# Performance work log

Measured on AMD Instinct MI355X. Metric: run time of the kernel, lower is better.

The kernel has to match this reference:

```python
import jax, jax.numpy as jnp
import numpy as np

EPS = 1e-8


def _layer_norm(x, w, b):
    mu = jnp.mean(x, axis=-1, keepdims=True)
    var = jnp.mean((x - mu) ** 2, axis=-1, keepdims=True)
    return (x - mu) * jax.lax.rsqrt(var + EPS) * w + b


def setup_inputs() -> dict:
    key = jax.random.key(0)
    k1, k2, k3 = jax.random.split(key, 3)
    B, S, D = 8, 2048, 1024
    return {
        "x_real": jax.random.normal(k1, (B, S, D), dtype=jnp.float32),
        "x_imag": jax.random.normal(k2, (B, S, D), dtype=jnp.float32),
        "phase_matrix": jax.random.normal(k3, (D, D), dtype=jnp.float32) * 0.02,
        "coherence_factor": jnp.ones((1,), dtype=jnp.float32) * 0.1,
        "ln_weight": jnp.ones((D,), dtype=jnp.float32),
        "ln_bias": jnp.zeros((D,), dtype=jnp.float32),
    }


def reference(x_real, x_imag, phase_matrix, coherence_factor, ln_weight, ln_bias):
    D = x_real.shape[-1]
    # coherence = mean_{i,j} cos(phi_i - phi_j) over the last dim pairwise;
    # exact trig identity: sum_{i,j} cos(phi_i-phi_j) = (sum cos)^2 + (sum sin)^2
    phases = jnp.arctan2(x_imag + EPS, x_real + EPS)          # [B,S,D]
    sc = jnp.sum(jnp.cos(phases), axis=-1, keepdims=True)      # [B,S,1]
    ss = jnp.sum(jnp.sin(phases), axis=-1, keepdims=True)      # [B,S,1]
    coherence = (sc * sc + ss * ss) / (D * D)                  # [B,S,1]

    # phase rotation driven by GEMM
    phase_adjustment = jnp.einsum('bsd,de->bse', x_real, phase_matrix)
    phase_adjustment = phase_adjustment * coherence_factor * (1.0 - coherence)
    c, s = jnp.cos(phase_adjustment), jnp.sin(phase_adjustment)
    new_real = x_real * c - x_imag * s
    new_imag = x_real * s + x_imag * c

    # unit-modulus normalization
    norm = jnp.sqrt(new_real ** 2 + new_imag ** 2 + EPS)
    new_real = new_real / norm
    new_imag = new_imag / norm

    return (_layer_norm(new_real, ln_weight, ln_bias),
            _layer_norm(new_imag, ln_weight, ln_bias))
```

## Files before the change

### kernel.cpp

```cpp
#include <hip/hip_runtime.h>
#include <hip/hip_fp16.h>

#define DEV __device__ __forceinline__

typedef __bf16 bf16x8 __attribute__((ext_vector_type(8)));
typedef float f32x4 __attribute__((ext_vector_type(4)));
typedef short s16x8 __attribute__((ext_vector_type(8)));
typedef unsigned short u16;

static constexpr int D = 1024;
static constexpr int M = 16384;
static constexpr int R = 32;
static constexpr float EPS = 1e-8f;
static constexpr int PAD = 1028;

static constexpr int SMEM_BYTES = 136192;
static constexpr int RED_OFF = 131584;
static constexpr int STATS_OFF = 135680;

DEV u16 f2bf(float f) {
  union { float f; unsigned u; } v; v.f = f;
  unsigned u = v.u;
  return (u16)((u + 0x7FFFu + ((u >> 16) & 1u)) >> 16);
}

union H2x4 { s16x8 v; __half2 h[4]; };

__global__ __launch_bounds__(256) void k_prep(const float* __restrict__ pm,
                                              u16* __restrict__ bt) {
  __shared__ float t[32][33];
  int bx = blockIdx.x * 32, by = blockIdx.y * 32;
  int tx = threadIdx.x, ty = threadIdx.y;
#pragma unroll
  for (int j = 0; j < 32; j += 8)
    t[ty + j][tx] = pm[(size_t)(by + ty + j) * D + bx + tx];
  __syncthreads();
#pragma unroll
  for (int j = 0; j < 32; j += 8) {
    int col = bx + ty + j, k = by + tx;
    int kk = k >> 5, nh = col >> 9, cb = (col >> 4) & 31, c15 = col & 15;
    int kg = (k >> 3) & 3, je = k & 7;
    bt[(size_t)(kk * 2 + nh) * 16384 + (size_t)((cb * 64 + kg * 16 + c15) * 8 + je)] =
        f2bf(t[tx][ty + j]);
  }
}

__global__ __launch_bounds__(512, 1) void k_fused(
    const float* __restrict__ xr, const float* __restrict__ xi,
    const u16* __restrict__ bt, const float* __restrict__ cfp,
    const float* __restrict__ lw, const float* __restrict__ lb,
    float* __restrict__ outR, float* __restrict__ outI) {
  __shared__ __align__(16) unsigned char smem[SMEM_BYTES];
  u16* A_lds = (u16*)smem;
  __half2* stash = (__half2*)smem;
  float* red = (float*)(smem + RED_OFF);
  float* stats = (float*)(smem + STATS_OFF);

  const int tid = threadIdx.x;
  const int lane = tid & 63;
  const int l15 = lane & 15, l4 = lane >> 4;
  const int wv = tid >> 6;
  const size_t row0 = (size_t)blockIdx.x * R;
  const float cfv = cfp[0];

  {
    int row = tid >> 4;
    int s16 = tid & 15;
    const float* src = xr + (row0 + row) * D;
#pragma unroll
    for (int it = 0; it < 4; ++it)
#pragma unroll
      for (int h = 0; h < 2; ++h) {
        int kgl = it * 32 + s16 * 2 + h;
        f32x4 a = *(const f32x4*)(src + kgl * 8);
        f32x4 b = *(const f32x4*)(src + kgl * 8 + 4);
        s16x8 v;
        v[0] = (short)f2bf(a.x); v[1] = (short)f2bf(a.y);
        v[2] = (short)f2bf(a.z); v[3] = (short)f2bf(a.w);
        v[4] = (short)f2bf(b.x); v[5] = (short)f2bf(b.y);
        v[6] = (short)f2bf(b.z); v[7] = (short)f2bf(b.w);
        int kk = kgl >> 2, kg = kgl & 3;
        int u = kk * 128 + (row >> 4) * 64 + kg * 16 + ((row & 15) ^ (kk & 15));
        *(s16x8*)&A_lds[u * 8] = v;
      }
  }
  __syncthreads();

  f32x4 acc[2][8] = {};

  auto loadA = [&](int kk, bf16x8 (&af)[2]) {
#pragma unroll
    for (int rb = 0; rb < 2; ++rb) {
      int u = kk * 128 + rb * 64 + l4 * 16 + (l15 ^ (kk & 15));
      af[rb] = __builtin_bit_cast(bf16x8, *(const s16x8*)&A_lds[u * 8]);
    }
  };
  auto loadB4 = [&](int s, bf16x8 (&b)[4]) {
    const u16* p = bt + (size_t)s * 16384 + (size_t)(wv * 4) * 512 + (size_t)lane * 8;
#pragma unroll
    for (int nf = 0; nf < 4; ++nf)
      b[nf] = __builtin_bit_cast(bf16x8, *(const s16x8*)(p + nf * 512));
  };
  auto step4 = [&](bf16x8 (&a)[2], bf16x8 (&b)[4], int nh) {
    __builtin_amdgcn_s_setprio(1);
#pragma unroll
    for (int nf = 0; nf < 4; ++nf) {
      acc[0][nh * 4 + nf] =
          __builtin_amdgcn_mfma_f32_16x16x32_bf16(a[0], b[nf], acc[0][nh * 4 + nf], 0, 0, 0);
      acc[1][nh * 4 + nf] =
          __builtin_amdgcn_mfma_f32_16x16x32_bf16(a[1], b[nf], acc[1][nh * 4 + nf], 0, 0, 0);
    }
    __builtin_amdgcn_s_setprio(0);
  };

  {
    bf16x8 a[2], b0v[4], b1v[4];
    loadB4(0, b0v);
    loadB4(1, b1v);
    for (int kk = 0; kk < 32; ++kk) {
      loadA(kk, a);
      step4(a, b0v, 0);
      if (kk < 31) loadB4(2 * kk + 2, b0v);
      step4(a, b1v, 1);
      if (kk < 31) loadB4(2 * kk + 3, b1v);
    }
  }
  __syncthreads();

  float sc8[8], ss8[8];
#pragma unroll
  for (int p = 0; p < 8; ++p) { sc8[p] = 0.f; ss8[p] = 0.f; }
#pragma unroll
  for (int rb = 0; rb < 2; ++rb)
#pragma unroll
    for (int i = 0; i < 4; ++i) {
      const int p = rb * 4 + i;
      const int row_l = rb * 16 + l4 * 4 + i;
      const float* ar = xr + (row0 + row_l) * D;
      const float* ai = xi + (row0 + row_l) * D;
#pragma unroll
      for (int q = 0; q < 8; ++q) {
        int col = (q >> 2) * 512 + wv * 64 + (q & 3) * 16 + l15;
        float a = ar[col], b = ai[col];
        float xe = a + EPS, ye = b + EPS;
        float inv = rsqrtf(xe * xe + ye * ye);
        sc8[p] += xe * inv;
        ss8[p] += ye * inv;
        stash[row_l * PAD + col] = __floats2half2_rn(a, b);
      }
    }
#pragma unroll
  for (int p = 0; p < 8; ++p)
#pragma unroll
    for (int d = 1; d < 16; d <<= 1) {
      sc8[p] += __shfl_xor(sc8[p], d, 64);
      ss8[p] += __shfl_xor(ss8[p], d, 64);
    }
  if (l15 == 0) {
#pragma unroll
    for (int rb = 0; rb < 2; ++rb)
#pragma unroll
      for (int i = 0; i < 4; ++i) {
        int p = rb * 4 + i, row_l = rb * 16 + l4 * 4 + i;
        red[(row_l * 8 + wv) * 4 + 0] = sc8[p];
        red[(row_l * 8 + wv) * 4 + 1] = ss8[p];
      }
  }
  __syncthreads();
  float srow[8];
#pragma unroll
  for (int rb = 0; rb < 2; ++rb)
#pragma unroll
    for (int i = 0; i < 4; ++i) {
      int p = rb * 4 + i, row_l = rb * 16 + l4 * 4 + i;
      float tsc = 0.f, tss = 0.f;
#pragma unroll
      for (int w8 = 0; w8 < 8; ++w8) {
        tsc += red[(row_l * 8 + w8) * 4 + 0];
        tss += red[(row_l * 8 + w8) * 4 + 1];
      }
      float coh = (tsc * tsc + tss * tss) * (1.0f / (1024.0f * 1024.0f));
      srow[p] = cfv * (1.0f - coh);
    }
  __syncthreads();

  float snr[8], sqr[8], sni[8], sqi[8];
#pragma unroll
  for (int p = 0; p < 8; ++p) { snr[p] = 0.f; sqr[p] = 0.f; sni[p] = 0.f; sqi[p] = 0.f; }
#pragma unroll
  for (int rb = 0; rb < 2; ++rb)
#pragma unroll
    for (int i = 0; i < 4; ++i) {
      const int p = rb * 4 + i;
      const int row_l = rb * 16 + l4 * 4 + i;
      const float sr = srow[p];
#pragma unroll
      for (int q = 0; q < 8; ++q) {
        int col = (q >> 2) * 512 + wv * 64 + (q & 3) * 16 + l15;
        float t = acc[rb][q][i] * sr;
        float t2 = t * t;
        float sn = t * (1.f + t2 * (-1.f / 6.f + t2 * (1.f / 120.f - t2 * (1.f / 5040.f))));
        float cs = 1.f + t2 * (-0.5f + t2 * (1.f / 24.f - t2 * (1.f / 720.f)));
        __half2 ab = stash[row_l * PAD + col];
        float a = __low2float(ab), b = __high2float(ab);
        float nr = a * cs - b * sn;
        float ni = a * sn + b * cs;
        float inv = rsqrtf(nr * nr + ni * ni + EPS);
        nr *= inv; ni *= inv;
        stash[row_l * PAD + col] = __floats2half2_rn(nr, ni);
        snr[p] += nr; sqr[p] += nr * nr;
        sni[p] += ni; sqi[p] += ni * ni;
      }
    }
#pragma unroll
  for (int p = 0; p < 8; ++p)
#pragma unroll
    for (int d = 1; d < 16; d <<= 1) {
      snr[p] += __shfl_xor(snr[p], d, 64);
      sqr[p] += __shfl_xor(sqr[p], d, 64);
      sni[p] += __shfl_xor(sni[p], d, 64);
      sqi[p] += __shfl_xor(sqi[p], d, 64);
    }
  if (l15 == 0) {
#pragma unroll
    for (int rb = 0; rb < 2; ++rb)
#pragma unroll
      for (int i = 0; i < 4; ++i) {
        int p = rb * 4 + i, row_l = rb * 16 + l4 * 4 + i;
        red[(row_l * 8 + wv) * 4 + 0] = snr[p];
        red[(row_l * 8 + wv) * 4 + 1] = sqr[p];
        red[(row_l * 8 + wv) * 4 + 2] = sni[p];
        red[(row_l * 8 + wv) * 4 + 3] = sqi[p];
      }
  }
  __syncthreads();
  if (wv == 0 && l15 == 0) {
#pragma unroll
    for (int rb = 0; rb < 2; ++rb)
#pragma unroll
      for (int i = 0; i < 4; ++i) {
        int row_l = rb * 16 + l4 * 4 + i;
        float s0 = 0.f, s1 = 0.f, s2 = 0.f, s3 = 0.f;
#pragma unroll
        for (int w8 = 0; w8 < 8; ++w8) {
          s0 += red[(row_l * 8 + w8) * 4 + 0];
          s1 += red[(row_l * 8 + w8) * 4 + 1];
          s2 += red[(row_l * 8 + w8) * 4 + 2];
          s3 += red[(row_l * 8 + w8) * 4 + 3];
        }
        float mu_r = s0 * (1.f / 1024.f);
        float mu_i = s2 * (1.f / 1024.f);
        stats[row_l * 4 + 0] = mu_r;
        stats[row_l * 4 + 1] = rsqrtf(s1 * (1.f / 1024.f) - mu_r * mu_r + EPS);
        stats[row_l * 4 + 2] = mu_i;
        stats[row_l * 4 + 3] = rsqrtf(s3 * (1.f / 1024.f) - mu_i * mu_i + EPS);
      }
  }
  __syncthreads();

  {
    int row = tid >> 4, cg = tid & 15;
    float mu_r = stats[row * 4 + 0], rd_r = stats[row * 4 + 1];
    float mu_i = stats[row * 4 + 2], rd_i = stats[row * 4 + 3];
    float* orp = outR + (row0 + row) * D;
    float* oip = outI + (row0 + row) * D;
#pragma unroll
    for (int v = 0; v < 16; ++v) {
      int col = v * 64 + cg * 4;
      H2x4 hv;
      hv.v = *(const s16x8*)&stash[row * PAD + col];
      f32x4 w4 = *(const f32x4*)(lw + col);
      f32x4 b4 = *(const f32x4*)(lb + col);
      f32x4 o_r, o_i;
#pragma unroll
      for (int j = 0; j < 4; ++j) {
        float nr = __low2float(hv.h[j]), ni = __high2float(hv.h[j]);
        o_r[j] = (nr - mu_r) * rd_r * w4[j] + b4[j];
        o_i[j] = (ni - mu_i) * rd_i * w4[j] + b4[j];
      }
      *(f32x4*)(orp + col) = o_r;
      *(f32x4*)(oip + col) = o_i;
    }
  }
}

extern "C" void kernel_launch(void* const* d_in, const int* in_sizes, int n_in,
                              void* d_out, int out_size, void* d_ws, size_t ws_size,
                              hipStream_t stream) {
  const float* xr = (const float*)d_in[0];
  const float* xi = (const float*)d_in[1];
  const float* pm = (const float*)d_in[2];
  const float* cf = (const float*)d_in[3];
  const float* lw = (const float*)d_in[4];
  const float* lb = (const float*)d_in[5];
  float* outR = (float*)d_out;
  float* outI = outR + (size_t)M * D;
  u16* bt = (u16*)d_ws;

  k_prep<<<dim3(32, 32), dim3(32, 8), 0, stream>>>(pm, bt);
  k_fused<<<M / R, 512, 0, stream>>>(xr, xi, bt, cf, lw, lb, outR, outI);
}
```

Before: 160.2 us.

## Halve row tile, stage B via async LDS loads, fuse coherence into A load

Shrinks the per-block row tile from 32 to 16 so LDS use drops to about 66KB, and raises launch bounds to allow several blocks per CU. The B operand is now copied cooperatively into shared memory with global_load_lds each k-step instead of being loaded straight into registers per wave. The coherence sums are computed while loading x for the bf16 A tile, so the separate fp16 stash pass over the inputs goes away; the stash now uses an XOR swizzle in place of padding. The cost is twice as many blocks each re-reading the full B matrix, and two barriers per half k-step with no double buffering of B.

```diff
diff --git a/kernel.cpp b/kernel.cpp
--- a/kernel.cpp
+++ b/kernel.cpp
@@ -10,18 +10,25 @@
 
 static constexpr int D = 1024;
 static constexpr int M = 16384;
-static constexpr int R = 32;
+static constexpr int R = 16;
 static constexpr float EPS = 1e-8f;
-static constexpr int PAD = 1028;
-
-static constexpr int SMEM_BYTES = 136192;
-static constexpr int RED_OFF = 131584;
-static constexpr int STATS_OFF = 135680;
+
+static constexpr int B_OFF = 32768;
+static constexpr int RED_OFF = 65536;
+static constexpr int STATS_OFF = 67584;
+static constexpr int SCALE_OFF = 67840;
+static constexpr int SMEM_BYTES = 67904;
 
 DEV u16 f2bf(float f) {
   union { float f; unsigned u; } v; v.f = f;
   unsigned u = v.u;
   return (u16)((u + 0x7FFFu + ((u >> 16) & 1u)) >> 16);
+}
+
+DEV void async_copy16(const void* g, void* l) {
+  __builtin_amdgcn_global_load_lds(
+      (const __attribute__((address_space(1))) void*)g,
+      (__attribute__((address_space(3))) void*)l, 16, 0, 0);
 }
 
 union H2x4 { s16x8 v; __half2 h[4]; };
@@ -45,16 +52,18 @@
   }
 }
 
-__global__ __launch_bounds__(512, 1) void k_fused(
+__global__ __launch_bounds__(512, 4) void k_fused(
     const float* __restrict__ xr, const float* __restrict__ xi,
     const u16* __restrict__ bt, const float* __restrict__ cfp,
     const float* __restrict__ lw, const float* __restrict__ lb,
     float* __restrict__ outR, float* __restrict__ outI) {
   __shared__ __align__(16) unsigned char smem[SMEM_BYTES];
   u16* A_lds = (u16*)smem;
+  u16* B_u16 = (u16*)(smem + B_OFF);
   __half2* stash = (__half2*)smem;
   float* red = (float*)(smem + RED_OFF);
   float* stats = (float*)(smem + STATS_OFF);
+  float* scale_s = (float*)(smem + SCALE_OFF);
 
   const int tid = threadIdx.x;
   const int lane = tid & 63;
@@ -64,211 +73,158 @@
   const float cfv = cfp[0];
 
   {
-    int row = tid >> 4;
-    int s16 = tid & 15;
-    const float* src = xr + (row0 + row) * D;
-#pragma unroll
-    for (int it = 0; it < 4; ++it)
-#pragma unroll
-      for (int h = 0; h < 2; ++h) {
-        int kgl = it * 32 + s16 * 2 + h;
-        f32x4 a = *(const f32x4*)(src + kgl * 8);
-        f32x4 b = *(const f32x4*)(src + kgl * 8 + 4);
-        s16x8 v;
-        v[0] = (short)f2bf(a.x); v[1] = (short)f2bf(a.y);
-        v[2] = (short)f2bf(a.z); v[3] = (short)f2bf(a.w);
-        v[4] = (short)f2bf(b.x); v[5] = (short)f2bf(b.y);
-        v[6] = (short)f2bf(b.z); v[7] = (short)f2bf(b.w);
-        int kk = kgl >> 2, kg = kgl & 3;
-        int u = kk * 128 + (row >> 4) * 64 + kg * 16 + ((row & 15) ^ (kk & 15));
-        *(s16x8*)&A_lds[u * 8] = v;
-      }
-  }
-  __syncthreads();
-
-  f32x4 acc[2][8] = {};
-
-  auto loadA = [&](int kk, bf16x8 (&af)[2]) {
-#pragma unroll
-    for (int rb = 0; rb < 2; ++rb) {
-      int u = kk * 128 + rb * 64 + l4 * 16 + (l15 ^ (kk & 15));
-      af[rb] = __builtin_bit_cast(bf16x8, *(const s16x8*)&A_lds[u * 8]);
-    }
-  };
-  auto loadB4 = [&](int s, bf16x8 (&b)[4]) {
-    const u16* p = bt + (size_t)s * 16384 + (size_t)(wv * 4) * 512 + (size_t)lane * 8;
-#pragma unroll
-    for (int nf = 0; nf < 4; ++nf)
-      b[nf] = __builtin_bit_cast(bf16x8, *(const s16x8*)(p + nf * 512));
-  };
-  auto step4 = [&](bf16x8 (&a)[2], bf16x8 (&b)[4], int nh) {
-    __builtin_amdgcn_s_setprio(1);
-#pragma unroll
-    for (int nf = 0; nf < 4; ++nf) {
-      acc[0][nh * 4 + nf] =
-          __builtin_amdgcn_mfma_f32_16x16x32_bf16(a[0], b[nf], acc[0][nh * 4 + nf], 0, 0, 0);
-      acc[1][nh * 4 + nf] =
-          __builtin_amdgcn_mfma_f32_16x16x32_bf16(a[1], b[nf], acc[1][nh * 4 + nf], 0, 0, 0);
-    }
-    __builtin_amdgcn_s_setprio(0);
-  };
+    int row = tid >> 5;
+    int s32 = tid & 31;
+    const float* xrp = xr + (row0 + row) * D;
+    const float* xip = xi + (row0 + row) * D;
+    float sc = 0.f, ss = 0.f;
+#pragma unroll
+    for (int it = 0; it < 4; ++it) {
+      int kgl = it * 32 + s32;
+      f32x4 a0 = *(const f32x4*)(xrp + kgl * 8);
+      f32x4 a1 = *(const f32x4*)(xrp + kgl * 8 + 4);
+      f32x4 b0 = *(const f32x4*)(xip + kgl * 8);
+      f32x4 b1 = *(const f32x4*)(xip + kgl * 8 + 4);
+      float fx[8] = {a0.x, a0.y, a0.z, a0.w, a1.x, a1.y, a1.z, a1.w};
+      float fy[8] = {b0.x, b0.y, b0.z, b0.w, b1.x, b1.y, b1.z, b1.w};
+      s16x8 v;
+#pragma unroll
+      for (int j = 0; j < 8; ++j) {
+        float x = fx[j] + EPS, y = fy[j] + EPS;
+        float inv = rsqrtf(x * x + y * y);
+        sc += x * inv;
+        ss += y * inv;
+        v[j] = (short)f2bf(fx[j]);
+      }
+      int kk = kgl >> 2, kg = kgl & 3;
+      int u = kk * 64 + kg * 16 + (row ^ (kk & 15));
+      *(s16x8*)&A_lds[u * 8] = v;
+    }
+    sc += __shfl_xor(sc, 1, 64); sc += __shfl_xor(sc, 2, 64);
+    sc += __shfl_xor(sc, 4, 64); sc += __shfl_xor(sc, 8, 64);
+    sc += __shfl_xor(sc, 16, 64);
+    ss += __shfl_xor(ss, 1, 64); ss += __shfl_xor(ss, 2, 64);
+    ss += __shfl_xor(ss, 4, 64); ss += __shfl_xor(ss, 8, 64);
+    ss += __shfl_xor(ss, 16, 64);
+    if (s32 == 0) {
+      float coh = (sc * sc + ss * ss) * (1.0f / (1024.0f * 1024.0f));
+      scale_s[row] = cfv * (1.0f - coh);
+    }
+  }
+  __syncthreads();
+
+  f32x4 acc[8] = {};
+
+  for (int kk = 0; kk < 32; ++kk) {
+    int ua = kk * 64 + l4 * 16 + (l15 ^ (kk & 15));
+    bf16x8 af = __builtin_bit_cast(bf16x8, *(const s16x8*)&A_lds[ua * 8]);
+#pragma unroll
+    for (int nh = 0; nh < 2; ++nh) {
+      const u16* src = bt + (size_t)(kk * 2 + nh) * 16384;
+#pragma unroll
+      for (int r = 0; r < 4; ++r) {
+        int off = (r * 8 + wv) * 512 + lane * 8;
+        async_copy16(src + off, B_u16 + off);
+      }
+      __syncthreads();
+      __builtin_amdgcn_s_setprio(1);
+#pragma unroll
+      for (int nf = 0; nf < 4; ++nf) {
+        int ub = (wv * 4 + nf) * 64 + l4 * 16 + l15;
+        bf16x8 bf = __builtin_bit_cast(bf16x8, *(const s16x8*)&B_u16[ub * 8]);
+        acc[nh * 4 + nf] =
+            __builtin_amdgcn_mfma_f32_16x16x32_bf16(af, bf, acc[nh * 4 + nf], 0, 0, 0);
+      }
+      __builtin_amdgcn_s_setprio(0);
+      __syncthreads();
+    }
+  }
+
+  float srow4[4];
+#pragma unroll
+  for (int i = 0; i < 4; ++i) srow4[i] = scale_s[l4 * 4 + i];
+
+  float s_r[4], q_r[4], s_i[4], q_i[4];
+#pragma unroll
+  for (int i = 0; i < 4; ++i) { s_r[i] = 0.f; q_r[i] = 0.f; s_i[i] = 0.f; q_i[i] = 0.f; }
+#pragma unroll
+  for (int i = 0; i < 4; ++i) {
+    const int row_l = l4 * 4 + i;
+    const float scl = srow4[i];
+    const float* ar = xr + (row0 + row_l) * D;
+    const float* ai = xi + (row0 + row_l) * D;
+#pragma unroll
+    for (int q = 0; q < 8; ++q) {
+      int col = (q >> 2) * 512 + wv * 64 + (q & 3) * 16 + l15;
+      float a = ar[col], b = ai[col];
+      float t = acc[q][i] * scl;
+      float t2 = t * t;
+      float sn = t * (1.f + t2 * (-1.f / 6.f + t2 * (1.f / 120.f - t2 * (1.f / 5040.f))));
+      float cs = 1.f + t2 * (-0.5f + t2 * (1.f / 24.f - t2 * (1.f / 720.f)));
+      float nr = a * cs - b * sn;
+      float ni = a * sn + b * cs;
+      float inv = rsqrtf(nr * nr + ni * ni + EPS);
+      nr *= inv; ni *= inv;
+      int colx = col ^ ((row_l & 3) << 4);
+      stash[row_l * 1024 + colx] = __floats2half2_rn(nr, ni);
+      s_r[i] += nr; q_r[i] += nr * nr;
+      s_i[i] += ni; q_i[i] += ni * ni;
+    }
+  }
+#pragma unroll
+  for (int i = 0; i < 4; ++i)
+#pragma unroll
+    for (int d = 1; d < 16; d <<= 1) {
+      s_r[i] += __shfl_xor(s_r[i], d, 64);
+      q_r[i] += __shfl_xor(q_r[i], d, 64);
+      s_i[i] += __shfl_xor(s_i[i], d, 64);
+      q_i[i] += __shfl_xor(q_i[i], d, 64);
+    }
+  if (l15 == 0) {
+#pragma unroll
+    for (int i = 0; i < 4; ++i) {
+      int row_l = l4 * 4 + i;
+      red[(row_l * 8 + wv) * 4 + 0] = s_r[i];
+      red[(row_l * 8 + wv) * 4 + 1] = q_r[i];
+      red[(row_l * 8 + wv) * 4 + 2] = s_i[i];
+      red[(row_l * 8 + wv) * 4 + 3] = q_i[i];
+    }
+  }
+  __syncthreads();
+  if (wv == 0 && l15 == 0) {
+#pragma unroll
+    for (int i = 0; i < 4; ++i) {
+      int row_l = l4 * 4 + i;
+      float s0 = 0.f, s1 = 0.f, s2 = 0.f, s3 = 0.f;
+#pragma unroll
+      for (int w8 = 0; w8 < 8; ++w8) {
+        s0 += red[(row_l * 8 + w8) * 4 + 0];
+        s1 += red[(row_l * 8 + w8) * 4 + 1];
+        s2 += red[(row_l * 8 + w8) * 4 + 2];
+        s3 += red[(row_l * 8 + w8) * 4 + 3];
+      }
+      float mu_r = s0 * (1.f / 1024.f);
+      float mu_i = s2 * (1.f / 1024.f);
+      stats[row_l * 4 + 0] = mu_r;
+      stats[row_l * 4 + 1] = rsqrtf(s1 * (1.f / 1024.f) - mu_r * mu_r + EPS);
+      stats[row_l * 4 + 2] = mu_i;
+      stats[row_l * 4 + 3] = rsqrtf(s3 * (1.f / 1024.f) - mu_i * mu_i + EPS);
+    }
+  }
+  __syncthreads();
 
   {
-    bf16x8 a[2], b0v[4], b1v[4];
-    loadB4(0, b0v);
-    loadB4(1, b1v);
-    for (int kk = 0; kk < 32; ++kk) {
-      loadA(kk, a);
-      step4(a, b0v, 0);
-      if (kk < 31) loadB4(2 * kk + 2, b0v);
-      step4(a, b1v, 1);
-      if (kk < 31) loadB4(2 * kk + 3, b1v);
-    }
-  }
-  __syncthreads();
-
-  float sc8[8], ss8[8];
-#pragma unroll
-  for (int p = 0; p < 8; ++p) { sc8[p] = 0.f; ss8[p] = 0.f; }
-#pragma unroll
-  for (int rb = 0; rb < 2; ++rb)
-#pragma unroll
-    for (int i = 0; i < 4; ++i) {
-      const int p = rb * 4 + i;
-      const int row_l = rb * 16 + l4 * 4 + i;
-      const float* ar = xr + (row0 + row_l) * D;
-      const float* ai = xi + (row0 + row_l) * D;
-#pragma unroll
-      for (int q = 0; q < 8; ++q) {
-        int col = (q >> 2) * 512 + wv * 64 + (q & 3) * 16 + l15;
-        float a = ar[col], b = ai[col];
-        float xe = a + EPS, ye = b + EPS;
-        float inv = rsqrtf(xe * xe + ye * ye);
-        sc8[p] += xe * inv;
-        ss8[p] += ye * inv;
-        stash[row_l * PAD + col] = __floats2half2_rn(a, b);
-      }
-    }
-#pragma unroll
-  for (int p = 0; p < 8; ++p)
-#pragma unroll
-    for (int d = 1; d < 16; d <<= 1) {
-      sc8[p] += __shfl_xor(sc8[p], d, 64);
-      ss8[p] += __shfl_xor(ss8[p], d, 64);
-    }
-  if (l15 == 0) {
-#pragma unroll
-    for (int rb = 0; rb < 2; ++rb)
-#pragma unroll
-      for (int i = 0; i < 4; ++i) {
-        int p = rb * 4 + i, row_l = rb * 16 + l4 * 4 + i;
-        red[(row_l * 8 + wv) * 4 + 0] = sc8[p];
-        red[(row_l * 8 + wv) * 4 + 1] = ss8[p];
-      }
-  }
-  __syncthreads();
-  float srow[8];
-#pragma unroll
-  for (int rb = 0; rb < 2; ++rb)
-#pragma unroll
-    for (int i = 0; i < 4; ++i) {
-      int p = rb * 4 + i, row_l = rb * 16 + l4 * 4 + i;
-      float tsc = 0.f, tss = 0.f;
-#pragma unroll
-      for (int w8 = 0; w8 < 8; ++w8) {
-        tsc += red[(row_l * 8 + w8) * 4 + 0];
-        tss += red[(row_l * 8 + w8) * 4 + 1];
-      }
-      float coh = (tsc * tsc + tss * tss) * (1.0f / (1024.0f * 1024.0f));
-      srow[p] = cfv * (1.0f - coh);
-    }
-  __syncthreads();
-
-  float snr[8], sqr[8], sni[8], sqi[8];
-#pragma unroll
-  for (int p = 0; p < 8; ++p) { snr[p] = 0.f; sqr[p] = 0.f; sni[p] = 0.f; sqi[p] = 0.f; }
-#pragma unroll
-  for (int rb = 0; rb < 2; ++rb)
-#pragma unroll
-    for (int i = 0; i < 4; ++i) {
-      const int p = rb * 4 + i;
-      const int row_l = rb * 16 + l4 * 4 + i;
-      const float sr = srow[p];
-#pragma unroll
-      for (int q = 0; q < 8; ++q) {
-        int col = (q >> 2) * 512 + wv * 64 + (q & 3) * 16 + l15;
-        float t = acc[rb][q][i] * sr;
-        float t2 = t * t;
-        float sn = t * (1.f + t2 * (-1.f / 6.f + t2 * (1.f / 120.f - t2 * (1.f / 5040.f))));
-        float cs = 1.f + t2 * (-0.5f + t2 * (1.f / 24.f - t2 * (1.f / 720.f)));
-        __half2 ab = stash[row_l * PAD + col];
-        float a = __low2float(ab), b = __high2float(ab);
-        float nr = a * cs - b * sn;
-        float ni = a * sn + b * cs;
-        float inv = rsqrtf(nr * nr + ni * ni + EPS);
-        nr *= inv; ni *= inv;
-        stash[row_l * PAD + col] = __floats2half2_rn(nr, ni);
-        snr[p] += nr; sqr[p] += nr * nr;
-        sni[p] += ni; sqi[p] += ni * ni;
-      }
-    }
-#pragma unroll
-  for (int p = 0; p < 8; ++p)
-#pragma unroll
-    for (int d = 1; d < 16; d <<= 1) {
-      snr[p] += __shfl_xor(snr[p], d, 64);
-      sqr[p] += __shfl_xor(sqr[p], d, 64);
-      sni[p] += __shfl_xor(sni[p], d, 64);
-      sqi[p] += __shfl_xor(sqi[p], d, 64);
-    }
-  if (l15 == 0) {
-#pragma unroll
-    for (int rb = 0; rb < 2; ++rb)
-#pragma unroll
-      for (int i = 0; i < 4; ++i) {
-        int p = rb * 4 + i, row_l = rb * 16 + l4 * 4 + i;
-        red[(row_l * 8 + wv) * 4 + 0] = snr[p];
-        red[(row_l * 8 + wv) * 4 + 1] = sqr[p];
-        red[(row_l * 8 + wv) * 4 + 2] = sni[p];
-        red[(row_l * 8 + wv) * 4 + 3] = sqi[p];
-      }
-  }
-  __syncthreads();
-  if (wv == 0 && l15 == 0) {
-#pragma unroll
-    for (int rb = 0; rb < 2; ++rb)
-#pragma unroll
-      for (int i = 0; i < 4; ++i) {
-        int row_l = rb * 16 + l4 * 4 + i;
-        float s0 = 0.f, s1 = 0.f, s2 = 0.f, s3 = 0.f;
-#pragma unroll
-        for (int w8 = 0; w8 < 8; ++w8) {
-          s0 += red[(row_l * 8 + w8) * 4 + 0];
-          s1 += red[(row_l * 8 + w8) * 4 + 1];
-          s2 += red[(row_l * 8 + w8) * 4 + 2];
-          s3 += red[(row_l * 8 + w8) * 4 + 3];
-        }
-        float mu_r = s0 * (1.f / 1024.f);
-        float mu_i = s2 * (1.f / 1024.f);
-        stats[row_l * 4 + 0] = mu_r;
-        stats[row_l * 4 + 1] = rsqrtf(s1 * (1.f / 1024.f) - mu_r * mu_r + EPS);
-        stats[row_l * 4 + 2] = mu_i;
-        stats[row_l * 4 + 3] = rsqrtf(s3 * (1.f / 1024.f) - mu_i * mu_i + EPS);
-      }
-  }
-  __syncthreads();
-
-  {
-    int row = tid >> 4, cg = tid & 15;
+    int row = tid >> 5, cg = tid & 31;
     float mu_r = stats[row * 4 + 0], rd_r = stats[row * 4 + 1];
     float mu_i = stats[row * 4 + 2], rd_i = stats[row * 4 + 3];
     float* orp = outR + (row0 + row) * D;
     float* oip = outI + (row0 + row) * D;
 #pragma unroll
-    for (int v = 0; v < 16; ++v) {
-      int col = v * 64 + cg * 4;
+    for (int v = 0; v < 8; ++v) {
+      int col = v * 128 + cg * 4;
+      int colx = col ^ ((row & 3) << 4);
       H2x4 hv;
-      hv.v = *(const s16x8*)&stash[row * PAD + col];
+      hv.v = *(const s16x8*)&stash[row * 1024 + colx];
       f32x4 w4 = *(const f32x4*)(lw + col);
       f32x4 b4 = *(const f32x4*)(lb + col);
       f32x4 o_r, o_i;
```

After: 150.3 us. 1.07x faster.
